# Kernel tuning notes

Measured on AMD Instinct MI355X. Metric: run time of the kernel, lower is better.

## Reference

```python
import jax, jax.numpy as jnp
import numpy as np

N_NODES = 50000
N_EDGES = 800000
F = 53
B = 128
H = 4


def _p(key, shape, scale=0.1):
    return jax.random.normal(key, shape, dtype=jnp.float32) * scale


def setup_inputs() -> dict:
    key = jax.random.key(0)
    ks = jax.random.split(key, 40)
    inp = {
        'x': jax.random.normal(ks[0], (N_NODES, F), dtype=jnp.float32),
        'edge_index': jax.random.randint(ks[1], (2, N_EDGES), 0, N_NODES),
        'batch': jnp.sort(jax.random.randint(ks[2], (N_NODES,), 0, B)),
        # GATConv(53 -> 53, heads=4)
        'gat_w': _p(ks[3], (F, H * F)),
        'gat_att_src': _p(ks[4], (H, F)),
        'gat_att_dst': _p(ks[5], (H, F)),
        'gat_bias': _p(ks[6], (H * F,)),
        # GINConv MLP: 53 -> 106 -> 106
        'gin_w1': _p(ks[7], (F, 2 * F)), 'gin_b1': _p(ks[8], (2 * F,)),
        'gin_w2': _p(ks[9], (2 * F, 2 * F)), 'gin_b2': _p(ks[10], (2 * F,)),
        # EdgeConv MLP: 106 -> 106 -> 106
        'ec_w1': _p(ks[11], (2 * F, 2 * F)), 'ec_b1': _p(ks[12], (2 * F,)),
        'ec_w2': _p(ks[13], (2 * F, 2 * F)), 'ec_b2': _p(ks[14], (2 * F,)),
        # per-branch heads
        'fg1_w': _p(ks[15], (4 * F, 256)), 'fg1_b': _p(ks[16], (256,)),
        'fg2_w': _p(ks[17], (256, 128)), 'fg2_b': _p(ks[18], (128,)),
        'fg3_w': _p(ks[19], (2 * F, 256)), 'fg3_b': _p(ks[20], (256,)),
        'fg4_w': _p(ks[21], (256, 128)), 'fg4_b': _p(ks[22], (128,)),
        'fg5_w': _p(ks[23], (2 * F, 256)), 'fg5_b': _p(ks[24], (256,)),
        'fg6_w': _p(ks[25], (256, 128)), 'fg6_b': _p(ks[26], (128,)),
        # final MLP
        'fc1_w': _p(ks[27], (384, 128)), 'fc1_b': _p(ks[28], (128,)),
        'fc2_w': _p(ks[29], (128, 64)), 'fc2_b': _p(ks[30], (64,)),
        'out_w': _p(ks[31], (64, 1)), 'out_b': _p(ks[32], (1,)),
    }
    return inp


def _gat(x, src, dst, w, a_src, a_dst, bias):
    # PyG GATConv with add_self_loops=True, negative_slope=0.2, concat heads
    n = x.shape[0]
    loop = jnp.arange(n)
    s = jnp.concatenate([src, loop])
    d = jnp.concatenate([dst, loop])
    xh = (x @ w).reshape(n, H, F)                      # [N,H,F]
    al_s = jnp.einsum('nhf,hf->nh', xh, a_src)         # [N,H]
    al_d = jnp.einsum('nhf,hf->nh', xh, a_dst)
    e = jax.nn.leaky_relu(al_s[s] + al_d[d], 0.2)      # [E2,H]
    m = jax.ops.segment_max(e, d, num_segments=n)
    ex = jnp.exp(e - m[d])
    z = jax.ops.segment_sum(ex, d, num_segments=n)
    alpha = ex / (z[d] + 1e-16)                        # softmax over in-edges
    msg = xh[s] * alpha[:, :, None]                    # [E2,H,F]
    out = jax.ops.segment_sum(msg, d, num_segments=n)
    return out.reshape(n, H * F) + bias


def _gin(x, src, dst, w1, b1, w2, b2):
    # PyG GINConv, eps=0: nn(x + sum_j x_j)
    n = x.shape[0]
    agg = jax.ops.segment_sum(x[src], dst, num_segments=n)
    h = x + agg
    return jax.nn.relu(h @ w1 + b1) @ w2 + b2


def _edgeconv(x, src, dst, w1, b1, w2, b2):
    # PyG EdgeConv: max_j nn([x_i, x_j - x_i]) at target i
    n = x.shape[0]
    xi = x[dst]
    feat = jnp.concatenate([xi, x[src] - xi], axis=-1)  # [E,2F]
    h = jax.nn.relu(feat @ w1 + b1) @ w2 + b2
    out = jax.ops.segment_max(h, dst, num_segments=n)
    return jnp.where(jnp.isfinite(out), out, 0.0)       # empty segments -> 0


def _gep(x, batch):
    # global mean pool per graph
    s = jax.ops.segment_sum(x, batch, num_segments=B)
    cnt = jax.ops.segment_sum(jnp.ones((x.shape[0],), x.dtype), batch, num_segments=B)
    return s / jnp.maximum(cnt, 1.0)[:, None]


def reference(x, edge_index, batch,
              gat_w, gat_att_src, gat_att_dst, gat_bias,
              gin_w1, gin_b1, gin_w2, gin_b2,
              ec_w1, ec_b1, ec_w2, ec_b2,
              fg1_w, fg1_b, fg2_w, fg2_b, fg3_w, fg3_b,
              fg4_w, fg4_b, fg5_w, fg5_b, fg6_w, fg6_b,
              fc1_w, fc1_b, fc2_w, fc2_b, out_w, out_b):
    relu = jax.nn.relu
    src, dst = edge_index[0], edge_index[1]

    xt = relu(_gat(x, src, dst, gat_w, gat_att_src, gat_att_dst, gat_bias))
    xt = _gep(xt, batch)
    xt = relu(xt @ fg1_w + fg1_b)
    xt = relu(xt @ fg2_w + fg2_b)

    xt2 = relu(_gin(x, src, dst, gin_w1, gin_b1, gin_w2, gin_b2))
    xt2 = _gep(xt2, batch)
    xt2 = relu(xt2 @ fg3_w + fg3_b)
    xt2 = relu(xt2 @ fg4_w + fg4_b)

    xt3 = relu(_edgeconv(x, src, dst, ec_w1, ec_b1, ec_w2, ec_b2))
    xt3 = _gep(xt3, batch)
    xt3 = relu(xt3 @ fg5_w + fg5_b)
    xt3 = relu(xt3 @ fg6_w + fg6_b)

    h = jnp.concatenate([xt, xt2, xt3], axis=1)         # [B,384]
    h = relu(h @ fc1_w + fc1_b)
    h = relu(h @ fc2_w + fc2_b)
    return jax.nn.sigmoid(h @ out_w + out_b)            # [B,1]
```

## Files before the change

kernel.cpp:

```cpp
#include <hip/hip_runtime.h>
#include <hip/hip_bf16.h>
#include <math.h>

#define N_NODES 50000
#define N_EDGES 800000
#define FDIM 53
#define BATCH 128
#define HF 212
#define F2 106
#define POOLW 424
#define NPK2 220
#define PSTR 32
#define ECS 128
#define A4P 256

typedef __attribute__((ext_vector_type(8))) short short8;
typedef __attribute__((ext_vector_type(4))) float f32x4;

__device__ __forceinline__ float leaky02(float x){ return x >= 0.f ? x : 0.2f * x; }

__device__ __forceinline__ short f2bf(float x) {
  unsigned u = __float_as_uint(x);
  unsigned r = (u + 0x7fffu + ((u >> 16) & 1u)) >> 16;
  return (short)r;
}
__device__ __forceinline__ float bf2f(short b) {
  return __uint_as_float(((unsigned)(unsigned short)b) << 16);
}
__device__ __forceinline__ unsigned pk2(float a, float b) {
  union { __hip_bfloat162 h; unsigned u; } c;
  c.h = __float22bfloat162_rn(make_float2(a, b));
  return c.u;
}
__device__ __forceinline__ void ldsbar() {
  __builtin_amdgcn_s_waitcnt(0xC07F);
  __builtin_amdgcn_s_barrier();
}

__global__ void k_prep(const float* __restrict__ ec_w1, const float* __restrict__ ec_b1,
                       const float* __restrict__ gat_w, const float* __restrict__ asrc,
                       const float* __restrict__ adst,
                       float* __restrict__ Wp, float* __restrict__ bp) {
  int idx = blockIdx.x * blockDim.x + threadIdx.x;
  if (idx < FDIM * NPK2) {
    int k = idx / NPK2, j = idx % NPK2;
    float v;
    if (j < F2)            v = ec_w1[k * F2 + j] - ec_w1[(FDIM + k) * F2 + j];
    else if (j < 2 * F2)   v = ec_w1[(FDIM + k) * F2 + (j - F2)];
    else {
      int r = j - 2 * F2;
      int sd = r >> 2, h = r & 3;
      const float* av = sd ? adst : asrc;
      float acc = 0.f;
      for (int f = 0; f < FDIM; ++f)
        acc += gat_w[k * HF + h * FDIM + f] * av[h * FDIM + f];
      v = acc;
    }
    Wp[idx] = v;
  }
  if (idx < NPK2) {
    bp[idx] = (idx < F2) ? ec_b1[idx] : 0.f;
  }
}

#define GM 64
#define GN 110
#define GNP 112
#define APAD 57
__global__ __launch_bounds__(256) void k_gemm(
    const float* __restrict__ x, const float* __restrict__ Wp, const float* __restrict__ bp,
    short* __restrict__ xb, short* __restrict__ Ub, short* __restrict__ Vb,
    float* __restrict__ alS, float* __restrict__ alD) {
  __shared__ float As[GM * APAD];
  __shared__ float Ws[FDIM * GNP];
  int mb = blockIdx.x >> 1, nc = blockIdx.x & 1;
  int m0 = mb * GM, n0 = nc * GN;
  int t = threadIdx.x;
  for (int idx = t; idx < GM * FDIM; idx += 256) {
    int m = idx / FDIM, k = idx % FDIM;
    int gm = m0 + m;
    float v = (gm < N_NODES) ? x[(size_t)gm * FDIM + k] : 0.f;
    As[m * APAD + k] = v;
    if (nc == 0 && gm < N_NODES) xb[(size_t)gm * 64 + k] = f2bf(v);
  }
  for (int idx = t; idx < FDIM * GNP; idx += 256) {
    int k = idx / GNP, n = idx % GNP;
    Ws[idx] = (n < GN) ? Wp[k * NPK2 + n0 + n] : 0.f;
  }
  __syncthreads();
  int tx = t & 15, ty = t >> 4;
  int ms = tx * 4, ns = ty * 7;
  float acc[4][7];
#pragma unroll
  for (int i = 0; i < 4; i++)
#pragma unroll
    for (int j = 0; j < 7; j++) acc[i][j] = 0.f;
  for (int k = 0; k < FDIM; k++) {
    float a0 = As[(ms + 0) * APAD + k];
    float a1 = As[(ms + 1) * APAD + k];
    float a2 = As[(ms + 2) * APAD + k];
    float a3 = As[(ms + 3) * APAD + k];
    float b[7];
#pragma unroll
    for (int j = 0; j < 7; j++) b[j] = Ws[k * GNP + ns + j];
#pragma unroll
    for (int j = 0; j < 7; j++) {
      acc[0][j] += a0 * b[j];
      acc[1][j] += a1 * b[j];
      acc[2][j] += a2 * b[j];
      acc[3][j] += a3 * b[j];
    }
  }
  float bj[7];
#pragma unroll
  for (int j = 0; j < 7; j++) {
    int g = n0 + ns + j;
    bj[j] = (g < NPK2) ? bp[g] : 0.f;
  }
#pragma unroll
  for (int i = 0; i < 4; i++) {
    int gm = m0 + ms + i;
    if (gm >= N_NODES) break;
#pragma unroll
    for (int j = 0; j < 7; j++) {
      int g = n0 + ns + j;
      float v = acc[i][j] + bj[j];
      if (g < F2)             Ub[(size_t)gm * ECS + g] = f2bf(v);
      else if (g < 2 * F2)    Vb[(size_t)gm * ECS + (g - F2)] = f2bf(v);
      else if (g < 2 * F2 + 4) alS[gm * 4 + (g - 2 * F2)] = v;
      else if (g < NPK2)      alD[gm * 4 + (g - 2 * F2 - 4)] = v;
    }
  }
}

#define SCAN_BLOCKS ((N_NODES + 255) / 256)

__global__ void k_hist(const int* __restrict__ ei, int* __restrict__ histP) {
  int t = blockIdx.x * blockDim.x + threadIdx.x;
  if (t < N_EDGES) atomicAdd(&histP[ei[N_EDGES + t] << 5], 1);
}

__global__ __launch_bounds__(256) void k_scan1(const int* __restrict__ histP,
                                               const int* __restrict__ batch,
                                               int* __restrict__ rp, int* __restrict__ bsum,
                                               int* __restrict__ start) {
  __shared__ int buf[256];
  int tid = threadIdx.x;
  int idx = blockIdx.x * 256 + tid;
  int v = (idx < N_NODES) ? histP[idx << 5] : 0;
  buf[tid] = v;
  __syncthreads();
  for (int off = 1; off < 256; off <<= 1) {
    int t2 = (tid >= off) ? buf[tid - off] : 0;
    __syncthreads();
    buf[tid] += t2;
    __syncthreads();
  }
  if (idx < N_NODES) rp[idx] = buf[tid] - v;
  if (tid == 255) bsum[blockIdx.x] = buf[255];
  if (idx < N_NODES) {
    int b = batch[idx];
    if (idx == 0)
      for (int g = 0; g <= b; g++) start[g] = 0;
    int bn = (idx + 1 < N_NODES) ? batch[idx + 1] : BATCH;
    for (int g = b + 1; g <= bn; g++) start[g] = idx + 1;
  }
}

__global__ __launch_bounds__(256) void k_scan3(const int* __restrict__ bsum,
                                               int* __restrict__ rp, int* __restrict__ histP) {
  __shared__ int buf[256];
  int tid = threadIdx.x;
  int v = (tid < SCAN_BLOCKS) ? bsum[tid] : 0;
  buf[tid] = v;
  __syncthreads();
  for (int off = 1; off < 256; off <<= 1) {
    int t2 = (tid >= off) ? buf[tid - off] : 0;
    __syncthreads();
    buf[tid] += t2;
    __syncthreads();
  }
  int boff = (blockIdx.x == 0) ? 0 : buf[blockIdx.x - 1];
  int idx = blockIdx.x * 256 + tid;
  if (idx < N_NODES) {
    int o = rp[idx] + boff;
    rp[idx] = o;
    histP[idx << 5] = o;
  }
  if (idx == 0) rp[N_NODES] = N_EDGES;
}

__global__ void k_scatter(const int* __restrict__ ei, int* __restrict__ histP,
                          int* __restrict__ colidx) {
  int e = blockIdx.x * blockDim.x + threadIdx.x;
  if (e >= N_EDGES) return;
  int d = ei[N_EDGES + e];
  int pos = atomicAdd(&histP[d << 5], 1);
  colidx[pos] = ei[e];
}

#define GCH 20
__global__ __launch_bounds__(256) void k_gatgin(
    const short* __restrict__ xb, const float* __restrict__ alS, const float* __restrict__ alD,
    const int* __restrict__ rp, const int* __restrict__ colidx,
    short* __restrict__ agg4, short* __restrict__ aggb) {
  int wid = threadIdx.x >> 6, lane = threadIdx.x & 63;
  bool fa = lane < FDIM;
  int i0 = blockIdx.x * GCH;
  int iend = min(i0 + GCH, N_NODES);
  __shared__ int rpG[GCH + 1];
  __shared__ int sL[4][64];
  __shared__ float4 eL[4][64];
  {
    int t = threadIdx.x, nn = iend - i0;
    if (t <= nn) rpG[t] = rp[i0 + t];
  }
  __syncthreads();
  for (int i = i0 + wid; i < iend; i += 4) {
    int base = rpG[i - i0], deg = rpG[i - i0 + 1] - base;
    float4 adv = *(const float4*)(alD + (size_t)i * 4);
    float4 asv = *(const float4*)(alS + (size_t)i * 4);
    float aldi[4] = {adv.x, adv.y, adv.z, adv.w};
    float exs[4];
    exs[0] = __expf(leaky02(asv.x + aldi[0]));
    exs[1] = __expf(leaky02(asv.y + aldi[1]));
    exs[2] = __expf(leaky02(asv.z + aldi[2]));
    exs[3] = __expf(leaky02(asv.w + aldi[3]));
    float xiv = fa ? bf2f(xb[(size_t)i * 64 + lane]) : 0.f;
    float ag0 = exs[0] * xiv, ag1 = exs[1] * xiv, ag2 = exs[2] * xiv, ag3 = exs[3] * xiv;
    float ax = xiv;
    float zl[4] = {0.f, 0.f, 0.f, 0.f};

    for (int c0 = 0; c0 < deg; c0 += 64) {
      int cn = min(64, deg - c0);
      int s = 0;
      float ex0 = 0.f, ex1 = 0.f, ex2 = 0.f, ex3 = 0.f;
      if (lane < cn) {
        s = colidx[base + c0 + lane];
        float4 av = *(const float4*)(alS + (size_t)s * 4);
        ex0 = __expf(leaky02(av.x + aldi[0]));
        ex1 = __expf(leaky02(av.y + aldi[1]));
        ex2 = __expf(leaky02(av.z + aldi[2]));
        ex3 = __expf(leaky02(av.w + aldi[3]));
        zl[0] += ex0; zl[1] += ex1; zl[2] += ex2; zl[3] += ex3;
      }
      sL[wid][lane] = s;
      eL[wid][lane] = make_float4(ex0, ex1, ex2, ex3);
      for (int jj = 0; jj < cn; jj += 4) {
        int4 s4 = *(const int4*)&sL[wid][jj];
        int sj[4] = {s4.x, s4.y, s4.z, s4.w};
        float4 e0 = eL[wid][jj + 0];
        float4 e1 = eL[wid][jj + 1];
        float4 e2 = eL[wid][jj + 2];
        float4 e3 = eL[wid][jj + 3];
        float xg[4];
#pragma unroll
        for (int q = 0; q < 4; q++)
          xg[q] = fa ? bf2f(xb[(size_t)sj[q] * 64 + lane]) : 0.f;
        ag0 += e0.x * xg[0] + e1.x * xg[1] + e2.x * xg[2] + e3.x * xg[3];
        ag1 += e0.y * xg[0] + e1.y * xg[1] + e2.y * xg[2] + e3.y * xg[3];
        ag2 += e0.z * xg[0] + e1.z * xg[1] + e2.z * xg[2] + e3.z * xg[3];
        ag3 += e0.w * xg[0] + e1.w * xg[1] + e2.w * xg[2] + e3.w * xg[3];
#pragma unroll
        for (int q = 0; q < 4; q++)
          if (jj + q < cn) ax += xg[q];
      }
    }
#pragma unroll
    for (int off = 32; off >= 1; off >>= 1)
#pragma unroll
      for (int h = 0; h < 4; h++) zl[h] += __shfl_xor(zl[h], off);
    {
      float z0 = zl[0] + exs[0] + 1e-16f;
      float z1 = zl[1] + exs[1] + 1e-16f;
      float z2 = zl[2] + exs[2] + 1e-16f;
      float z3 = zl[3] + exs[3] + 1e-16f;
      short* ar = agg4 + (size_t)i * A4P;
      ar[0 * 64 + lane] = fa ? f2bf(ag0 / z0) : (short)0;
      ar[1 * 64 + lane] = fa ? f2bf(ag1 / z1) : (short)0;
      ar[2 * 64 + lane] = fa ? f2bf(ag2 / z2) : (short)0;
      ar[3 * 64 + lane] = fa ? f2bf(ag3 / z3) : (short)0;
      float axv = fa ? ax : 0.f;
      short hi = f2bf(axv);
      float lov = axv - bf2f(hi);
      short* br = aggb + (size_t)i * 128;
      br[lane]      = fa ? hi : (short)0;
      br[64 + lane] = fa ? f2bf(lov) : (short)0;
    }
  }
}

#define BTS 72
__global__ __launch_bounds__(256) void k_gt(
    const short* __restrict__ agg4, const float* __restrict__ gat_w,
    const float* __restrict__ gat_b, const int* __restrict__ batch,
    float* __restrict__ pooled) {
  __shared__ short Bt[4 * 56 * BTS];
  __shared__ float psum[4 * 224];
  __shared__ int batL[64];
  int m0 = blockIdx.x * 64;
  int t = threadIdx.x;
  for (int idx = t; idx < 4 * 224; idx += 256) psum[idx] = 0.f;
  if (t < 64) batL[t] = batch[min(m0 + t, N_NODES - 1)];
  for (int idx = t; idx < 4 * 64 * 56; idx += 256) {
    int n = idx % 56, kk = (idx / 56) & 63, h = idx / (56 * 64);
    short v = (kk < FDIM && n < FDIM) ? f2bf(gat_w[kk * HF + h * FDIM + n]) : (short)0;
    Bt[(h * 56 + n) * BTS + kk] = v;
  }
  __syncthreads();
  const int lane = t & 63, wid = t >> 6;
  const int n16 = lane & 15, quad = lane >> 4;
  const int mrow0 = wid * 16;
  const int bmin = batL[0];
  const bool uni = (batL[0] == batL[63]);
  const size_t abase = (size_t)(m0 + mrow0 + n16) * A4P;
#pragma unroll
  for (int h = 0; h < 4; h++) {
    short8 af0 = *(const short8*)(agg4 + abase + h * 64 + quad * 8);
    short8 af1 = *(const short8*)(agg4 + abase + h * 64 + 32 + quad * 8);
#pragma unroll
    for (int nt = 0; nt < 4; nt++) {
      short8 b0 = *(const short8*)&Bt[(h * 56 + nt * 16 + n16) * BTS + quad * 8];
      short8 b1 = *(const short8*)&Bt[(h * 56 + nt * 16 + n16) * BTS + 32 + quad * 8];
      f32x4 acc = {0.f, 0.f, 0.f, 0.f};
      acc = __builtin_amdgcn_mfma_f32_16x16x32_bf16(af0, b0, acc, 0, 0, 0);
      acc = __builtin_amdgcn_mfma_f32_16x16x32_bf16(af1, b1, acc, 0, 0, 0);
      int jn = nt * 16 + n16;
      bool jv = jn < FDIM;
      float bj = jv ? gat_b[h * FDIM + jn] : 0.f;
      if (uni) {
        float s = 0.f;
#pragma unroll
        for (int r = 0; r < 4; r++) {
          int gm = m0 + mrow0 + quad * 4 + r;
          if (gm < N_NODES) s += fmaxf(acc[r] + bj, 0.f);
        }
        s += __shfl_xor(s, 16);
        s += __shfl_xor(s, 32);
        if (quad == 0 && jv && s != 0.f) atomicAdd(&psum[h * 56 + jn], s);
      } else {
        float pj = 0.f; int curb = -1;
#pragma unroll
        for (int r = 0; r < 4; r++) {
          int lm = mrow0 + quad * 4 + r;
          int gm = m0 + lm;
          if (gm < N_NODES) {
            float o = fmaxf(acc[r] + bj, 0.f);
            int b = batL[lm];
            if (b != curb) {
              if (curb >= 0 && jv) {
                int slot = curb - bmin;
                if (slot >= 0 && slot < 4) atomicAdd(&psum[slot * 224 + h * 56 + jn], pj);
                else atomicAdd(&pooled[(size_t)curb * POOLW + h * FDIM + jn], pj);
              }
              curb = b; pj = o;
            } else {
              pj += o;
            }
          }
        }
        if (curb >= 0 && jv) {
          int slot = curb - bmin;
          if (slot >= 0 && slot < 4) atomicAdd(&psum[slot * 224 + h * 56 + jn], pj);
          else atomicAdd(&pooled[(size_t)curb * POOLW + h * FDIM + jn], pj);
        }
      }
    }
  }
  __syncthreads();
  for (int idx = t; idx < 4 * 224; idx += 256) {
    int slot = idx / 224, c = idx % 224;
    int h = c / 56, jn = c % 56;
    float v = psum[idx];
    int b = bmin + slot;
    if (jn < FDIM && b < BATCH && v != 0.f)
      atomicAdd(&pooled[(size_t)b * POOLW + h * FDIM + jn], v);
  }
}

#define H1S 132
#define BWS 132
__global__ __launch_bounds__(256) void k_ginm(
    const short* __restrict__ aggb,
    const float* __restrict__ w1, const float* __restrict__ b1,
    const float* __restrict__ w2, const float* __restrict__ b2,
    const int* __restrict__ batch, float* __restrict__ pooled) {
  __shared__ short h1hi[64 * H1S];
  __shared__ short h1lo[64 * H1S];
  __shared__ short Btw[112 * BWS];
  __shared__ float psum[4 * 112];
  __shared__ int batL[64];
  int m0 = blockIdx.x * 64;
  int t = threadIdx.x;
  for (int idx = t; idx < 4 * 112; idx += 256) psum[idx] = 0.f;
  if (t < 64) batL[t] = batch[min(m0 + t, N_NODES - 1)];
  for (int idx = t; idx < 64 * H1S / 2; idx += 256) {
    ((int*)h1hi)[idx] = 0;
    ((int*)h1lo)[idx] = 0;
  }
  for (int idx = t; idx < 112 * 128; idx += 256) {
    int n = idx >> 7, kk = idx & 127;
    int ks = kk & 63;
    short v = (ks < FDIM && n < F2) ? f2bf(w1[ks * F2 + n]) : (short)0;
    Btw[n * BWS + kk] = v;
  }
  __syncthreads();
  const int lane = t & 63, wid = t >> 6;
  const int n16 = lane & 15, quad = lane >> 4;
  const int mrow0 = wid * 16;
  const int bmin = batL[0];
  const bool uni = (batL[0] == batL[63]);
  {
    const size_t abase = (size_t)(m0 + mrow0 + n16) * 128;
    short8 a[4];
#pragma unroll
    for (int f = 0; f < 4; f++)
      a[f] = *(const short8*)(aggb + abase + f * 32 + quad * 8);
#pragma unroll
    for (int nt = 0; nt < 7; nt++) {
      f32x4 acc = {0.f, 0.f, 0.f, 0.f};
#pragma unroll
      for (int f = 0; f < 4; f++) {
        short8 bf = *(const short8*)&Btw[(nt * 16 + n16) * BWS + f * 32 + quad * 8];
        acc = __builtin_amdgcn_mfma_f32_16x16x32_bf16(a[f], bf, acc, 0, 0, 0);
      }
      int jn = nt * 16 + n16;
      if (jn < F2) {
        float bj = b1[jn];
#pragma unroll
        for (int r = 0; r < 4; r++) {
          int row = mrow0 + quad * 4 + r;
          float v = fmaxf(acc[r] + bj, 0.f);
          short hi = f2bf(v);
          h1hi[row * H1S + jn] = hi;
          h1lo[row * H1S + jn] = f2bf(v - bf2f(hi));
        }
      }
    }
  }
  __syncthreads();
  for (int idx = t; idx < 112 * 128; idx += 256) {
    int n = idx >> 7, kk = idx & 127;
    short v = (kk < F2 && n < F2) ? f2bf(w2[kk * F2 + n]) : (short)0;
    Btw[n * BWS + kk] = v;
  }
  __syncthreads();
  short8 ah[4], al[4];
#pragma unroll
  for (int f = 0; f < 4; f++) {
    ah[f] = *(const short8*)&h1hi[(mrow0 + n16) * H1S + f * 32 + quad * 8];
    al[f] = *(const short8*)&h1lo[(mrow0 + n16) * H1S + f * 32 + quad * 8];
  }
#pragma unroll
  for (int nt = 0; nt < 7; nt++) {
    f32x4 acc = {0.f, 0.f, 0.f, 0.f};
#pragma unroll
    for (int f = 0; f < 4; f++) {
      short8 bf = *(const short8*)&Btw[(nt * 16 + n16) * BWS + f * 32 + quad * 8];
      acc = __builtin_amdgcn_mfma_f32_16x16x32_bf16(ah[f], bf, acc, 0, 0, 0);
      acc = __builtin_amdgcn_mfma_f32_16x16x32_bf16(al[f], bf, acc, 0, 0, 0);
    }
    int jn = nt * 16 + n16;
    bool jv = jn < F2;
    float bj = jv ? b2[jn] : 0.f;
    if (uni) {
      float s = 0.f;
#pragma unroll
      for (int r = 0; r < 4; r++) {
        int gm = m0 + mrow0 + quad * 4 + r;
        if (gm < N_NODES) s += fmaxf(acc[r] + bj, 0.f);
      }
      s += __shfl_xor(s, 16);
      s += __shfl_xor(s, 32);
      if (quad == 0 && jv && s != 0.f) atomicAdd(&psum[jn], s);
    } else {
      float pj = 0.f; int curb = -1;
#pragma unroll
      for (int r = 0; r < 4; r++) {
        int lm = mrow0 + quad * 4 + r;
        int gm = m0 + lm;
        if (gm < N_NODES) {
          float o = fmaxf(acc[r] + bj, 0.f);
          int b = batL[lm];
          if (b != curb) {
            if (curb >= 0 && jv) {
              int slot = curb - bmin;
              if (slot >= 0 && slot < 4) atomicAdd(&psum[slot * 112 + jn], pj);
              else atomicAdd(&pooled[(size_t)curb * POOLW + HF + jn], pj);
            }
            curb = b; pj = o;
          } else {
            pj += o;
          }
        }
      }
      if (curb >= 0 && jv) {
        int slot = curb - bmin;
        if (slot >= 0 && slot < 4) atomicAdd(&psum[slot * 112 + jn], pj);
        else atomicAdd(&pooled[(size_t)curb * POOLW + HF + jn], pj);
      }
    }
  }
  __syncthreads();
  for (int idx = t; idx < 4 * 112; idx += 256) {
    int slot = idx / 112, n = idx % 112;
    float v = psum[idx];
    int b = bmin + slot;
    if (n < F2 && b < BATCH && v != 0.f)
      atomicAdd(&pooled[(size_t)b * POOLW + HF + n], v);
  }
}

#define ECH 25
__global__ __launch_bounds__(256) void k_ec(
    const short* __restrict__ Ub, const short* __restrict__ Vb,
    const float* __restrict__ w2, const float* __restrict__ b2,
    const int* __restrict__ rp, const int* __restrict__ colidx,
    const int* __restrict__ batch, float* __restrict__ pooled) {
  const int t = threadIdx.x;
  const int lane = t & 63, wid = t >> 6;
  const int n16 = lane & 15, quad = lane >> 4;
  const int nt = (wid == 3) ? 1 : 2;

  const int i0 = blockIdx.x * ECH;
  const int iend = min(i0 + ECH, N_NODES);
  const int nn = iend - i0;

  __shared__ int rpL[ECH + 1];
  __shared__ int batL[ECH];

  short8 Bh[2][4];
  for (int tt = 0; tt < 2; tt++) {
    int ucol = (wid * 2 + tt) * 16 + n16;
    for (int kc = 0; kc < 4; kc++) {
      short8 vh;
#pragma unroll
      for (int jv = 0; jv < 8; jv++) {
        int kk = kc * 32 + quad * 8 + jv;
        float w = (ucol < F2 && kk < F2) ? w2[kk * F2 + ucol] : 0.f;
        vh[jv] = f2bf(w);
      }
      Bh[tt][kc] = vh;
    }
  }
  float b2v[2];
#pragma unroll
  for (int tt = 0; tt < 2; tt++) {
    int u = (wid * 2 + tt) * 16 + n16;
    b2v[tt] = (u < F2) ? b2[u] : 0.f;
  }

  if (t <= nn) rpL[t] = rp[i0 + t];
  if (t < nn) batL[t] = batch[i0 + t];
  __syncthreads();

  __shared__ short hs[2][16 * 16 * 8];
  union SU { short8 s; unsigned u[4]; };
  const int es = t & 15, kg = t >> 4;
  const int k0 = kg * 8;

  float sm0 = 0.f, sm1 = 0.f;
  int curb = -1;
  const int u0 = (wid * 2) * 16 + n16;
  const int u1 = (wid * 2 + 1) * 16 + n16;

  auto advance = [&](int& ii, int& ttb, int& bb, int& dd) -> bool {
    ttb++;
    if (ttb * 16 < dd) return true;
    ttb = 0;
    for (ii = ii + 1; ii < iend; ii++) {
      bb = rpL[ii - i0]; dd = rpL[ii - i0 + 1] - bb;
      if (dd > 0) return true;
    }
    return false;
  };

  int i = i0, tb = 0, base = 0, deg = 0;
  bool have = false;
  for (; i < iend; i++) {
    base = rpL[i - i0]; deg = rpL[i - i0 + 1] - base;
    if (deg > 0) { have = true; break; }
  }
  short8 pu8{}, pv8{};
  int i1 = i, tb1 = 0, base1 = base, deg1 = deg;
  bool have1 = false;
  int sc = 0;
  if (have) {
    pu8 = *(const short8*)(Ub + (size_t)i * ECS + k0);
    int s0 = colidx[base + ((es < deg) ? es : 0)];
    pv8 = *(const short8*)(Vb + (size_t)s0 * ECS + k0);
    have1 = advance(i1, tb1, base1, deg1);
    if (have1) {
      int eg = tb1 * 16 + es;
      sc = colidx[base1 + ((eg < deg1) ? eg : 0)];
    }
  }

  float Uc[8];
  float vmax0 = -1e30f, vmax1 = -1e30f;
  int parity = 0;
  while (have) {
    if (tb == 0) {
#pragma unroll
      for (int j = 0; j < 8; j++) Uc[j] = bf2f(pu8[j]);
    }
    SU w;
#pragma unroll
    for (int p = 0; p < 4; p++) {
      bool kv = (k0 + 2 * p) < F2;
      float h0 = kv ? fmaxf(Uc[2 * p]     + bf2f(pv8[2 * p]),     0.f) : 0.f;
      float h1 = kv ? fmaxf(Uc[2 * p + 1] + bf2f(pv8[2 * p + 1]), 0.f) : 0.f;
      w.u[p] = pk2(h0, h1);
    }
    *(short8*)&hs[parity][(kg * 16 + es) * 8] = w.s;

    int i2 = i1, tb2 = tb1, base2 = base1, deg2 = deg1;
    bool have2 = false;
    int scN = 0;
    if (have1) {
      if (tb1 == 0) pu8 = *(const short8*)(Ub + (size_t)i1 * ECS + k0);
      pv8 = *(const short8*)(Vb + (size_t)sc * ECS + k0);
      have2 = advance(i2, tb2, base2, deg2);
      if (have2) {
        int eg2 = tb2 * 16 + es;
        scN = colidx[base2 + ((eg2 < deg2) ? eg2 : 0)];
      }
    }

    ldsbar();
    f32x4 a0 = {0.f, 0.f, 0.f, 0.f}, a1 = {0.f, 0.f, 0.f, 0.f};
#pragma unroll
    for (int kc = 0; kc < 4; kc++) {
      short8 af = *(const short8*)&hs[parity][((kc * 4 + quad) * 16 + n16) * 8];
      a0 = __builtin_amdgcn_mfma_f32_16x16x32_bf16(af, Bh[0][kc], a0, 0, 0, 0);
      if (nt > 1)
        a1 = __builtin_amdgcn_mfma_f32_16x16x32_bf16(af, Bh[1][kc], a1, 0, 0, 0);
    }
#pragma unroll
    for (int r = 0; r < 4; r++) {
      int er = tb * 16 + quad * 4 + r;
      if (er < deg) { vmax0 = fmaxf(vmax0, a0[r]); vmax1 = fmaxf(vmax1, a1[r]); }
    }
    if (!have1 || i1 != i) {
      vmax0 = fmaxf(vmax0, __shfl_xor(vmax0, 16));
      vmax0 = fmaxf(vmax0, __shfl_xor(vmax0, 32));
      vmax1 = fmaxf(vmax1, __shfl_xor(vmax1, 16));
      vmax1 = fmaxf(vmax1, __shfl_xor(vmax1, 32));
      float o0 = fmaxf(vmax0 + b2v[0], 0.f);
      float o1 = fmaxf(vmax1 + b2v[1], 0.f);
      int b = batL[i - i0];
      if (b != curb) {
        if (curb >= 0 && quad == 0) {
          float* pg = pooled + (size_t)curb * POOLW + HF + F2;
          if (u0 < F2) atomicAdd(&pg[u0], sm0);
          if (nt > 1 && u1 < F2) atomicAdd(&pg[u1], sm1);
        }
        curb = b; sm0 = o0; sm1 = o1;
      } else {
        sm0 += o0; sm1 += o1;
      }
      vmax0 = -1e30f; vmax1 = -1e30f;
    }
    i = i1; tb = tb1; base = base1; deg = deg1; have = have1;
    i1 = i2; tb1 = tb2; base1 = base2; deg1 = deg2; have1 = have2;
    sc = scN;
    parity ^= 1;
  }
  if (curb >= 0 && quad == 0) {
    float* pg = pooled + (size_t)curb * POOLW + HF + F2;
    if (u0 < F2) atomicAdd(&pg[u0], sm0);
    if (nt > 1 && u1 < F2) atomicAdd(&pg[u1], sm1);
  }
}

__global__ __launch_bounds__(256) void k_heads(
    const float* __restrict__ pooled, const int* __restrict__ start,
    const float* __restrict__ fg1_w, const float* __restrict__ fg1_b,
    const float* __restrict__ fg2_w, const float* __restrict__ fg2_b,
    const float* __restrict__ fg3_w, const float* __restrict__ fg3_b,
    const float* __restrict__ fg4_w, const float* __restrict__ fg4_b,
    const float* __restrict__ fg5_w, const float* __restrict__ fg5_b,
    const float* __restrict__ fg6_w, const float* __restrict__ fg6_b,
    const float* __restrict__ fc1_w, const float* __restrict__ fc1_b,
    const float* __restrict__ fc2_w, const float* __restrict__ fc2_b,
    const float* __restrict__ out_w, const float* __restrict__ out_b,
    float* __restrict__ out) {
  int g = blockIdx.x, t = threadIdx.x;
  __shared__ float in[POOLW];
  __shared__ float mid[256];
  __shared__ float cat[384];
  __shared__ float h1[128];
  __shared__ float h2[64];
  float c = fmaxf((float)(start[g + 1] - start[g]), 1.f);
  for (int idx = t; idx < POOLW; idx += 256)
    in[idx] = pooled[(size_t)g * POOLW + idx] / c;
  __syncthreads();
  const float* w1s[3] = {fg1_w, fg3_w, fg5_w};
  const float* b1s[3] = {fg1_b, fg3_b, fg5_b};
  const float* w2s[3] = {fg2_w, fg4_w, fg6_w};
  const float* b2s[3] = {fg2_b, fg4_b, fg6_b};
  const int off[4] = {0, HF, HF + F2, POOLW};
  for (int br = 0; br < 3; br++) {
    int kin = off[br + 1] - off[br];
    const float* iv = &in[off[br]];
    float a = b1s[br][t];
    const float* W = w1s[br];
    for (int k = 0; k < kin; k++) a += iv[k] * W[k * 256 + t];
    mid[t] = fmaxf(a, 0.f);
    __syncthreads();
    if (t < 128) {
      float b = b2s[br][t];
      const float* W2 = w2s[br];
      for (int k = 0; k < 256; k++) b += mid[k] * W2[k * 128 + t];
      cat[br * 128 + t] = fmaxf(b, 0.f);
    }
    __syncthreads();
  }
  if (t < 128) {
    float a = fc1_b[t];
    for (int k = 0; k < 384; k++) a += cat[k] * fc1_w[k * 128 + t];
    h1[t] = fmaxf(a, 0.f);
  }
  __syncthreads();
  if (t < 64) {
    float a = fc2_b[t];
    for (int k = 0; k < 128; k++) a += h1[k] * fc2_w[k * 64 + t];
    h2[t] = fmaxf(a, 0.f);
  }
  __syncthreads();
  if (t == 0) {
    float a = out_b[0];
    for (int k = 0; k < 64; k++) a += h2[k] * out_w[k];
    out[g] = 1.f / (1.f + __expf(-a));
  }
}

extern "C" void kernel_launch(void* const* d_in, const int* in_sizes, int n_in,
                              void* d_out, int out_size, void* d_ws, size_t ws_size,
                              hipStream_t stream) {
  const float* x      = (const float*)d_in[0];
  const int*   ei     = (const int*)d_in[1];
  const int*   batch  = (const int*)d_in[2];
  const float* gat_w  = (const float*)d_in[3];
  const float* asrc   = (const float*)d_in[4];
  const float* adst   = (const float*)d_in[5];
  const float* gat_b  = (const float*)d_in[6];
  const float* gin_w1 = (const float*)d_in[7];
  const float* gin_b1 = (const float*)d_in[8];
  const float* gin_w2 = (const float*)d_in[9];
  const float* gin_b2 = (const float*)d_in[10];
  const float* ec_w1  = (const float*)d_in[11];
  const float* ec_b1  = (const float*)d_in[12];
  const float* ec_w2  = (const float*)d_in[13];
  const float* ec_b2  = (const float*)d_in[14];
  const float* fg1_w = (const float*)d_in[15]; const float* fg1_b = (const float*)d_in[16];
  const float* fg2_w = (const float*)d_in[17]; const float* fg2_b = (const float*)d_in[18];
  const float* fg3_w = (const float*)d_in[19]; const float* fg3_b = (const float*)d_in[20];
  const float* fg4_w = (const float*)d_in[21]; const float* fg4_b = (const float*)d_in[22];
  const float* fg5_w = (const float*)d_in[23]; const float* fg5_b = (const float*)d_in[24];
  const float* fg6_w = (const float*)d_in[25]; const float* fg6_b = (const float*)d_in[26];
  const float* fc1_w = (const float*)d_in[27]; const float* fc1_b = (const float*)d_in[28];
  const float* fc2_w = (const float*)d_in[29]; const float* fc2_b = (const float*)d_in[30];
  const float* out_w = (const float*)d_in[31]; const float* out_b = (const float*)d_in[32];
  float* out = (float*)d_out;

  char* ws = (char*)d_ws;
  size_t off = 0;
  auto alloc = [&](size_t bytes) -> void* {
    void* p = ws + off;
    off = (off + bytes + 255) & ~(size_t)255;
    return p;
  };
  size_t zoff0 = off;
  int*   histP  = (int*)alloc((size_t)N_NODES * PSTR * sizeof(int));
  float* pooled = (float*)alloc((size_t)BATCH * POOLW * sizeof(float));
  size_t zbytes = off - zoff0;
  int*   rp     = (int*)alloc((N_NODES + 1) * sizeof(int));
  int*   start  = (int*)alloc((BATCH + 1) * sizeof(int));
  int*   bsum   = (int*)alloc(256 * sizeof(int));
  int*   colidx = (int*)alloc(N_EDGES * sizeof(int));
  short* xb     = (short*)alloc((size_t)N_NODES * 64 * sizeof(short));
  float* alS    = (float*)alloc((size_t)N_NODES * 4 * sizeof(float));
  float* alD    = (float*)alloc((size_t)N_NODES * 4 * sizeof(float));
  short* Ubuf   = (short*)alloc((size_t)N_NODES * ECS * sizeof(short));
  short* Vbuf   = (short*)alloc((size_t)N_NODES * ECS * sizeof(short));
  short* agg4   = (short*)alloc((size_t)(N_NODES + 64) * A4P * sizeof(short));
  short* aggb   = (short*)alloc((size_t)(N_NODES + 64) * 128 * sizeof(short));
  float* Wp     = (float*)alloc((size_t)FDIM * NPK2 * sizeof(float));
  float* bpk    = (float*)alloc(NPK2 * sizeof(float));
  (void)ws_size; (void)in_sizes; (void)n_in; (void)out_size;

  hipMemsetAsync(ws + zoff0, 0, zbytes, stream);

  k_prep<<<(FDIM * NPK2 + 255) / 256, 256, 0, stream>>>(ec_w1, ec_b1, gat_w, asrc, adst,
                                                        Wp, bpk);
  k_gemm<<<((N_NODES + GM - 1) / GM) * 2, 256, 0, stream>>>(x, Wp, bpk,
                                                            xb, Ubuf, Vbuf, alS, alD);
  k_hist<<<(N_EDGES + 255) / 256, 256, 0, stream>>>(ei, histP);
  k_scan1<<<SCAN_BLOCKS, 256, 0, stream>>>(histP, batch, rp, bsum, start);
  k_scan3<<<SCAN_BLOCKS, 256, 0, stream>>>(bsum, rp, histP);
  k_scatter<<<(N_EDGES + 255) / 256, 256, 0, stream>>>(ei, histP, colidx);

  k_gatgin<<<(N_NODES + GCH - 1) / GCH, 256, 0, stream>>>(xb, alS, alD, rp, colidx,
                                                          agg4, aggb);
  k_ec<<<(N_NODES + ECH - 1) / ECH, 256, 0, stream>>>(Ubuf, Vbuf, ec_w2, ec_b2, rp, colidx, batch, pooled);
  k_gt<<<(N_NODES + 63) / 64, 256, 0, stream>>>(agg4, gat_w, gat_b, batch, pooled);
  k_ginm<<<(N_NODES + 63) / 64, 256, 0, stream>>>(aggb, gin_w1, gin_b1, gin_w2, gin_b2,
                                                  batch, pooled);

  k_heads<<<BATCH, 256, 0, stream>>>(pooled, start,
                                     fg1_w, fg1_b, fg2_w, fg2_b, fg3_w, fg3_b,
                                     fg4_w, fg4_b, fg5_w, fg5_b, fg6_w, fg6_b,
                                     fc1_w, fc1_b, fc2_w, fc2_b, out_w, out_b, out);
}
```

Measured before the change: 634.7 us.

## Replace fp32 node GEMM with split-bf16 MFMA and precompute packed weights once

```diff
diff --git a/kernel.cpp b/kernel.cpp
--- a/kernel.cpp
+++ b/kernel.cpp
@@ -9,7 +9,6 @@
 #define HF 212
 #define F2 106
 #define POOLW 424
-#define NPK2 220
 #define PSTR 32
 #define ECS 128
 #define A4P 256
@@ -37,98 +36,116 @@
   __builtin_amdgcn_s_barrier();
 }
 
-__global__ void k_prep(const float* __restrict__ ec_w1, const float* __restrict__ ec_b1,
-                       const float* __restrict__ gat_w, const float* __restrict__ asrc,
-                       const float* __restrict__ adst,
-                       float* __restrict__ Wp, float* __restrict__ bp) {
+#define SEG_CAL 424
+#define SEG_WGT (4*56*64)
+#define SEG_WUV (2*112*256)
+#define SEG_WG1 (112*128)
+#define SEG_WG2 (112*128)
+#define PREP_TOT (SEG_CAL + SEG_WGT + SEG_WUV + SEG_WG1 + SEG_WG2)
+__global__ void k_prep(const float* __restrict__ gat_w, const float* __restrict__ asrc,
+                       const float* __restrict__ adst, const float* __restrict__ ec_w1,
+                       const float* __restrict__ gin_w1, const float* __restrict__ gin_w2,
+                       float* __restrict__ cAl, short* __restrict__ Wgt,
+                       short* __restrict__ Wuv, short* __restrict__ Wg1,
+                       short* __restrict__ Wg2) {
   int idx = blockIdx.x * blockDim.x + threadIdx.x;
-  if (idx < FDIM * NPK2) {
-    int k = idx / NPK2, j = idx % NPK2;
-    float v;
-    if (j < F2)            v = ec_w1[k * F2 + j] - ec_w1[(FDIM + k) * F2 + j];
-    else if (j < 2 * F2)   v = ec_w1[(FDIM + k) * F2 + (j - F2)];
-    else {
-      int r = j - 2 * F2;
-      int sd = r >> 2, h = r & 3;
-      const float* av = sd ? adst : asrc;
-      float acc = 0.f;
-      for (int f = 0; f < FDIM; ++f)
-        acc += gat_w[k * HF + h * FDIM + f] * av[h * FDIM + f];
-      v = acc;
-    }
-    Wp[idx] = v;
-  }
-  if (idx < NPK2) {
-    bp[idx] = (idx < F2) ? ec_b1[idx] : 0.f;
-  }
-}
-
-#define GM 64
-#define GN 110
-#define GNP 112
-#define APAD 57
-__global__ __launch_bounds__(256) void k_gemm(
-    const float* __restrict__ x, const float* __restrict__ Wp, const float* __restrict__ bp,
-    short* __restrict__ xb, short* __restrict__ Ub, short* __restrict__ Vb,
-    float* __restrict__ alS, float* __restrict__ alD) {
-  __shared__ float As[GM * APAD];
-  __shared__ float Ws[FDIM * GNP];
-  int mb = blockIdx.x >> 1, nc = blockIdx.x & 1;
-  int m0 = mb * GM, n0 = nc * GN;
+  if (idx < SEG_CAL) {
+    int k = idx >> 3, r = idx & 7, sd = r >> 2, h = r & 3;
+    const float* av = sd ? adst : asrc;
+    float acc = 0.f;
+    for (int f = 0; f < FDIM; ++f)
+      acc += gat_w[k * HF + h * FDIM + f] * av[h * FDIM + f];
+    cAl[idx] = acc;
+    return;
+  }
+  idx -= SEG_CAL;
+  if (idx < SEG_WGT) {
+    int h = idx / (56 * 64), rem = idx % (56 * 64);
+    int n = rem >> 6, kk = rem & 63;
+    Wgt[idx] = (kk < FDIM && n < FDIM) ? f2bf(gat_w[kk * HF + h * FDIM + n]) : (short)0;
+    return;
+  }
+  idx -= SEG_WGT;
+  if (idx < SEG_WUV) {
+    int c = idx / (112 * 256), rem = idx % (112 * 256);
+    int n = rem >> 8, kk = rem & 255, ks = kk & 63;
+    float w = 0.f;
+    if (ks < FDIM && n < F2)
+      w = (c == 0) ? ec_w1[ks * F2 + n] - ec_w1[(FDIM + ks) * F2 + n]
+                   : ec_w1[(FDIM + ks) * F2 + n];
+    short hv = f2bf(w);
+    Wuv[idx] = (kk < 128) ? hv : f2bf(w - bf2f(hv));
+    return;
+  }
+  idx -= SEG_WUV;
+  if (idx < SEG_WG1) {
+    int n = idx >> 7, kk = idx & 127, ks = kk & 63;
+    Wg1[idx] = (ks < FDIM && n < F2) ? f2bf(gin_w1[ks * F2 + n]) : (short)0;
+    return;
+  }
+  idx -= SEG_WG1;
+  if (idx < SEG_WG2) {
+    int n = idx >> 7, kk = idx & 127;
+    Wg2[idx] = (kk < F2 && n < F2) ? f2bf(gin_w2[kk * F2 + n]) : (short)0;
+  }
+}
+
+__global__ __launch_bounds__(256) void k_xsplit(
+    const float* __restrict__ x, const float* __restrict__ cAl,
+    short* __restrict__ xbhl, float* __restrict__ alS, float* __restrict__ alD) {
+  int wid = threadIdx.x >> 6, lane = threadIdx.x & 63;
+  int i = blockIdx.x * 4 + wid;
+  if (i >= N_NODES) return;
+  float v = (lane < FDIM) ? x[(size_t)i * FDIM + lane] : 0.f;
+  short hi = f2bf(v);
+  xbhl[(size_t)i * 128 + lane] = hi;
+  xbhl[(size_t)i * 128 + 64 + lane] = f2bf(v - bf2f(hi));
+  float out = 0.f;
+#pragma unroll
+  for (int j = 0; j < 8; j++) {
+    float p = (lane < FDIM) ? v * cAl[lane * 8 + j] : 0.f;
+#pragma unroll
+    for (int off = 32; off >= 1; off >>= 1) p += __shfl_xor(p, off);
+    if (lane == j) out = p;
+  }
+  if (lane < 4) alS[i * 4 + lane] = out;
+  else if (lane < 8) alD[i * 4 + (lane - 4)] = out;
+}
+
+__global__ __launch_bounds__(256) void k_uv(
+    const short* __restrict__ xbhl, const short* __restrict__ Wuv,
+    const float* __restrict__ ec_b1,
+    short* __restrict__ Ub, short* __restrict__ Vb) {
+  int bid = blockIdx.x;
+  int nb = bid >> 1, c = bid & 1;
+  int m0 = nb * 64;
   int t = threadIdx.x;
-  for (int idx = t; idx < GM * FDIM; idx += 256) {
-    int m = idx / FDIM, k = idx % FDIM;
-    int gm = m0 + m;
-    float v = (gm < N_NODES) ? x[(size_t)gm * FDIM + k] : 0.f;
-    As[m * APAD + k] = v;
-    if (nc == 0 && gm < N_NODES) xb[(size_t)gm * 64 + k] = f2bf(v);
-  }
-  for (int idx = t; idx < FDIM * GNP; idx += 256) {
-    int k = idx / GNP, n = idx % GNP;
-    Ws[idx] = (n < GN) ? Wp[k * NPK2 + n0 + n] : 0.f;
-  }
-  __syncthreads();
-  int tx = t & 15, ty = t >> 4;
-  int ms = tx * 4, ns = ty * 7;
-  float acc[4][7];
-#pragma unroll
-  for (int i = 0; i < 4; i++)
-#pragma unroll
-    for (int j = 0; j < 7; j++) acc[i][j] = 0.f;
-  for (int k = 0; k < FDIM; k++) {
-    float a0 = As[(ms + 0) * APAD + k];
-    float a1 = As[(ms + 1) * APAD + k];
-    float a2 = As[(ms + 2) * APAD + k];
-    float a3 = As[(ms + 3) * APAD + k];
-    float b[7];
-#pragma unroll
-    for (int j = 0; j < 7; j++) b[j] = Ws[k * GNP + ns + j];
-#pragma unroll
-    for (int j = 0; j < 7; j++) {
-      acc[0][j] += a0 * b[j];
-      acc[1][j] += a1 * b[j];
-      acc[2][j] += a2 * b[j];
-      acc[3][j] += a3 * b[j];
-    }
-  }
-  float bj[7];
-#pragma unroll
-  for (int j = 0; j < 7; j++) {
-    int g = n0 + ns + j;
-    bj[j] = (g < NPK2) ? bp[g] : 0.f;
-  }
-#pragma unroll
-  for (int i = 0; i < 4; i++) {
-    int gm = m0 + ms + i;
-    if (gm >= N_NODES) break;
-#pragma unroll
-    for (int j = 0; j < 7; j++) {
-      int g = n0 + ns + j;
-      float v = acc[i][j] + bj[j];
-      if (g < F2)             Ub[(size_t)gm * ECS + g] = f2bf(v);
-      else if (g < 2 * F2)    Vb[(size_t)gm * ECS + (g - F2)] = f2bf(v);
-      else if (g < 2 * F2 + 4) alS[gm * 4 + (g - 2 * F2)] = v;
-      else if (g < NPK2)      alD[gm * 4 + (g - 2 * F2 - 4)] = v;
+  const int lane = t & 63, wid = t >> 6;
+  const int n16 = lane & 15, quad = lane >> 4;
+  const int mrow0 = wid * 16;
+  const size_t abase = (size_t)(m0 + mrow0 + n16) * 128;
+  short8 a[4];
+#pragma unroll
+  for (int f = 0; f < 4; f++)
+    a[f] = *(const short8*)(xbhl + abase + f * 32 + quad * 8);
+  const short* Bw = Wuv + (size_t)c * 112 * 256;
+  short* Ob = c ? Vb : Ub;
+#pragma unroll
+  for (int nt = 0; nt < 7; nt++) {
+    f32x4 acc = {0.f, 0.f, 0.f, 0.f};
+#pragma unroll
+    for (int f = 0; f < 8; f++) {
+      short8 bf = *(const short8*)(Bw + (nt * 16 + n16) * 256 + f * 32 + quad * 8);
+      acc = __builtin_amdgcn_mfma_f32_16x16x32_bf16(a[f & 3], bf, acc, 0, 0, 0);
+    }
+    int jn = nt * 16 + n16;
+    if (jn < F2) {
+      float bj = c ? 0.f : ec_b1[jn];
+#pragma unroll
+      for (int r = 0; r < 4; r++) {
+        int gm = m0 + mrow0 + quad * 4 + r;
+        if (gm < N_NODES) Ob[(size_t)gm * ECS + jn] = f2bf(acc[r] + bj);
+      }
     }
   }
 }
@@ -201,7 +218,7 @@
 
 #define GCH 20
 __global__ __launch_bounds__(256) void k_gatgin(
-    const short* __restrict__ xb, const float* __restrict__ alS, const float* __restrict__ alD,
+    const short* __restrict__ xbhl, const float* __restrict__ alS, const float* __restrict__ alD,
     const int* __restrict__ rp, const int* __restrict__ colidx,
     short* __restrict__ agg4, short* __restrict__ aggb) {
   int wid = threadIdx.x >> 6, lane = threadIdx.x & 63;
@@ -226,7 +243,7 @@
     exs[1] = __expf(leaky02(asv.y + aldi[1]));
     exs[2] = __expf(leaky02(asv.z + aldi[2]));
     exs[3] = __expf(leaky02(asv.w + aldi[3]));
-    float xiv = fa ? bf2f(xb[(size_t)i * 64 + lane]) : 0.f;
+    float xiv = fa ? bf2f(xbhl[(size_t)i * 128 + lane]) : 0.f;
     float ag0 = exs[0] * xiv, ag1 = exs[1] * xiv, ag2 = exs[2] * xiv, ag3 = exs[3] * xiv;
     float ax = xiv;
     float zl[4] = {0.f, 0.f, 0.f, 0.f};
@@ -256,7 +273,7 @@
         float xg[4];
 #pragma unroll
         for (int q = 0; q < 4; q++)
-          xg[q] = fa ? bf2f(xb[(size_t)sj[q] * 64 + lane]) : 0.f;
+          xg[q] = fa ? bf2f(xbhl[(size_t)sj[q] * 128 + lane]) : 0.f;
         ag0 += e0.x * xg[0] + e1.x * xg[1] + e2.x * xg[2] + e3.x * xg[3];
         ag1 += e0.y * xg[0] + e1.y * xg[1] + e2.y * xg[2] + e3.y * xg[3];
         ag2 += e0.z * xg[0] + e1.z * xg[1] + e2.z * xg[2] + e3.z * xg[3];
@@ -290,23 +307,16 @@
   }
 }
 
-#define BTS 72
 __global__ __launch_bounds__(256) void k_gt(
-    const short* __restrict__ agg4, const float* __restrict__ gat_w,
+    const short* __restrict__ agg4, const short* __restrict__ Wgt,
     const float* __restrict__ gat_b, const int* __restrict__ batch,
     float* __restrict__ pooled) {
-  __shared__ short Bt[4 * 56 * BTS];
   __shared__ float psum[4 * 224];
   __shared__ int batL[64];
   int m0 = blockIdx.x * 64;
   int t = threadIdx.x;
   for (int idx = t; idx < 4 * 224; idx += 256) psum[idx] = 0.f;
   if (t < 64) batL[t] = batch[min(m0 + t, N_NODES - 1)];
-  for (int idx = t; idx < 4 * 64 * 56; idx += 256) {
-    int n = idx % 56, kk = (idx / 56) & 63, h = idx / (56 * 64);
-    short v = (kk < FDIM && n < FDIM) ? f2bf(gat_w[kk * HF + h * FDIM + n]) : (short)0;
-    Bt[(h * 56 + n) * BTS + kk] = v;
-  }
   __syncthreads();
   const int lane = t & 63, wid = t >> 6;
   const int n16 = lane & 15, quad = lane >> 4;
@@ -320,8 +330,8 @@
     short8 af1 = *(const short8*)(agg4 + abase + h * 64 + 32 + quad * 8);
 #pragma unroll
     for (int nt = 0; nt < 4; nt++) {
-      short8 b0 = *(const short8*)&Bt[(h * 56 + nt * 16 + n16) * BTS + quad * 8];
-      short8 b1 = *(const short8*)&Bt[(h * 56 + nt * 16 + n16) * BTS + 32 + quad * 8];
+      short8 b0 = *(const short8*)(Wgt + (h * 56 + nt * 16 + n16) * 64 + quad * 8);
+      short8 b1 = *(const short8*)(Wgt + (h * 56 + nt * 16 + n16) * 64 + 32 + quad * 8);
       f32x4 acc = {0.f, 0.f, 0.f, 0.f};
       acc = __builtin_amdgcn_mfma_f32_16x16x32_bf16(af0, b0, acc, 0, 0, 0);
       acc = __builtin_amdgcn_mfma_f32_16x16x32_bf16(af1, b1, acc, 0, 0, 0);
@@ -379,15 +389,13 @@
 }
 
 #define H1S 132
-#define BWS 132
 __global__ __launch_bounds__(256) void k_ginm(
-    const short* __restrict__ aggb,
-    const float* __restrict__ w1, const float* __restrict__ b1,
-    const float* __restrict__ w2, const float* __restrict__ b2,
+    const short* __restrict__ aggb, const short* __restrict__ Wg1,
+    const short* __restrict__ Wg2,
+    const float* __restrict__ b1, const float* __restrict__ b2,
     const int* __restrict__ batch, float* __restrict__ pooled) {
   __shared__ short h1hi[64 * H1S];
   __shared__ short h1lo[64 * H1S];
-  __shared__ short Btw[112 * BWS];
   __shared__ float psum[4 * 112];
   __shared__ int batL[64];
   int m0 = blockIdx.x * 64;
@@ -398,12 +406,6 @@
     ((int*)h1hi)[idx] = 0;
     ((int*)h1lo)[idx] = 0;
   }
-  for (int idx = t; idx < 112 * 128; idx += 256) {
-    int n = idx >> 7, kk = idx & 127;
-    int ks = kk & 63;
-    short v = (ks < FDIM && n < F2) ? f2bf(w1[ks * F2 + n]) : (short)0;
-    Btw[n * BWS + kk] = v;
-  }
   __syncthreads();
   const int lane = t & 63, wid = t >> 6;
   const int n16 = lane & 15, quad = lane >> 4;
@@ -421,7 +423,7 @@
       f32x4 acc = {0.f, 0.f, 0.f, 0.f};
 #pragma unroll
       for (int f = 0; f < 4; f++) {
-        short8 bf = *(const short8*)&Btw[(nt * 16 + n16) * BWS + f * 32 + quad * 8];
+        short8 bf = *(const short8*)(Wg1 + (nt * 16 + n16) * 128 + f * 32 + quad * 8);
         acc = __builtin_amdgcn_mfma_f32_16x16x32_bf16(a[f], bf, acc, 0, 0, 0);
       }
       int jn = nt * 16 + n16;
@@ -439,12 +441,6 @@
     }
   }
   __syncthreads();
-  for (int idx = t; idx < 112 * 128; idx += 256) {
-    int n = idx >> 7, kk = idx & 127;
-    short v = (kk < F2 && n < F2) ? f2bf(w2[kk * F2 + n]) : (short)0;
-    Btw[n * BWS + kk] = v;
-  }
-  __syncthreads();
   short8 ah[4], al[4];
 #pragma unroll
   for (int f = 0; f < 4; f++) {
@@ -456,7 +452,7 @@
     f32x4 acc = {0.f, 0.f, 0.f, 0.f};
 #pragma unroll
     for (int f = 0; f < 4; f++) {
-      short8 bf = *(const short8*)&Btw[(nt * 16 + n16) * BWS + f * 32 + quad * 8];
+      short8 bf = *(const short8*)(Wg2 + (nt * 16 + n16) * 128 + f * 32 + quad * 8);
       acc = __builtin_amdgcn_mfma_f32_16x16x32_bf16(ah[f], bf, acc, 0, 0, 0);
       acc = __builtin_amdgcn_mfma_f32_16x16x32_bf16(al[f], bf, acc, 0, 0, 0);
     }
@@ -779,33 +775,37 @@
   int*   start  = (int*)alloc((BATCH + 1) * sizeof(int));
   int*   bsum   = (int*)alloc(256 * sizeof(int));
   int*   colidx = (int*)alloc(N_EDGES * sizeof(int));
-  short* xb     = (short*)alloc((size_t)N_NODES * 64 * sizeof(short));
+  short* xbhl   = (short*)alloc((size_t)(N_NODES + 64) * 128 * sizeof(short));
   float* alS    = (float*)alloc((size_t)N_NODES * 4 * sizeof(float));
   float* alD    = (float*)alloc((size_t)N_NODES * 4 * sizeof(float));
   short* Ubuf   = (short*)alloc((size_t)N_NODES * ECS * sizeof(short));
   short* Vbuf   = (short*)alloc((size_t)N_NODES * ECS * sizeof(short));
   short* agg4   = (short*)alloc((size_t)(N_NODES + 64) * A4P * sizeof(short));
   short* aggb   = (short*)alloc((size_t)(N_NODES + 64) * 128 * sizeof(short));
-  float* Wp     = (float*)alloc((size_t)FDIM * NPK2 * sizeof(float));
-  float* bpk    = (float*)alloc(NPK2 * sizeof(float));
+  float* cAl    = (float*)alloc(SEG_CAL * sizeof(float));
+  short* Wgt    = (short*)alloc(SEG_WGT * sizeof(short));
+  short* Wuv    = (short*)alloc(SEG_WUV * sizeof(short));
+  short* Wg1    = (short*)alloc(SEG_WG1 * sizeof(short));
+  short* Wg2    = (short*)alloc(SEG_WG2 * sizeof(short));
   (void)ws_size; (void)in_sizes; (void)n_in; (void)out_size;
 
   hipMemsetAsync(ws + zoff0, 0, zbytes, stream);
 
-  k_prep<<<(FDIM * NPK2 + 255) / 256, 256, 0, stream>>>(ec_w1, ec_b1, gat_w, asrc, adst,
-                                                        Wp, bpk);
-  k_gemm<<<((N_NODES + GM - 1) / GM) * 2, 256, 0, stream>>>(x, Wp, bpk,
-                                                            xb, Ubuf, Vbuf, alS, alD);
+  k_prep<<<(PREP_TOT + 255) / 256, 256, 0, stream>>>(gat_w, asrc, adst, ec_w1,
+                                                     gin_w1, gin_w2,
+                                                     cAl, Wgt, Wuv, Wg1, Wg2);
+  k_xsplit<<<(N_NODES + 3) / 4, 256, 0, stream>>>(x, cAl, xbhl, alS, alD);
+  k_uv<<<((N_NODES + 63) / 64) * 2, 256, 0, stream>>>(xbhl, Wuv, ec_b1, Ubuf, Vbuf);
   k_hist<<<(N_EDGES + 255) / 256, 256, 0, stream>>>(ei, histP);
   k_scan1<<<SCAN_BLOCKS, 256, 0, stream>>>(histP, batch, rp, bsum, start);
   k_scan3<<<SCAN_BLOCKS, 256, 0, stream>>>(bsum, rp, histP);
   k_scatter<<<(N_EDGES + 255) / 256, 256, 0, stream>>>(ei, histP, colidx);
 
-  k_gatgin<<<(N_NODES + GCH - 1) / GCH, 256, 0, stream>>>(xb, alS, alD, rp, colidx,
+  k_gatgin<<<(N_NODES + GCH - 1) / GCH, 256, 0, stream>>>(xbhl, alS, alD, rp, colidx,
                                                           agg4, aggb);
   k_ec<<<(N_NODES + ECH - 1) / ECH, 256, 0, stream>>>(Ubuf, Vbuf, ec_w2, ec_b2, rp, colidx, batch, pooled);
-  k_gt<<<(N_NODES + 63) / 64, 256, 0, stream>>>(agg4, gat_w, gat_b, batch, pooled);
-  k_ginm<<<(N_NODES + 63) / 64, 256, 0, stream>>>(aggb, gin_w1, gin_b1, gin_w2, gin_b2,
+  k_gt<<<(N_NODES + 63) / 64, 256, 0, stream>>>(agg4, Wgt, gat_b, batch, pooled);
+  k_ginm<<<(N_NODES + 63) / 64, 256, 0, stream>>>(aggb, Wg1, Wg2, gin_b1, gin_b2,
                                                   batch, pooled);
 
   k_heads<<<BATCH, 256, 0, stream>>>(pooled, start,
```

Result: faster. 614.2 us (-3.2%).
